# Kernel tuning notes

Measured on AMD Instinct MI355X. Metric: run time of the kernel, lower is better.

The kernel has to match this reference:

```python
import jax, jax.numpy as jnp
import numpy as np

E, L, R, H, V = 8, 8, 4, 4096, 32000
B, S = 2, 1024


def setup_inputs() -> dict:
    key = jax.random.key(0)
    ks = jax.random.split(key, 8)
    scale = 0.02
    return {
        "hidden_state": jax.random.normal(ks[0], (B, S, H), jnp.float32),
        "router_w": jax.random.normal(ks[1], (E, H), jnp.float32) * scale,
        "router_b": jnp.zeros((E,), jnp.float32),
        "expert_B": jax.random.normal(ks[2], (E, L, R, H), jnp.float32) * scale,
        "expert_A": jax.random.normal(ks[3], (E, L, H, R), jnp.float32) * scale,
        "deep_B": jax.random.normal(ks[4], (L, R, H), jnp.float32) * scale,
        "deep_A": jax.random.normal(ks[5], (L, H, R), jnp.float32) * scale,
        "lm_head_w": jax.random.normal(ks[6], (V, H), jnp.float32) * scale,
    }


def reference(hidden_state, router_w, router_b, expert_B, expert_A,
              deep_B, deep_A, lm_head_w):
    h = hidden_state  # [B,S,H]
    # Router applies softmax internally; forward softmaxes AGAIN (faithful to source).
    router_logits = jax.nn.softmax(
        jnp.einsum('bsh,eh->bse', h, router_w) + router_b, axis=-1)
    router_probs = jax.nn.softmax(router_logits, axis=-1)  # [B,S,E]
    psum = jnp.sum(router_probs, axis=-1, keepdims=True)   # [B,S,1] (== 1)

    n_layers = deep_B.shape[0]
    for i in range(n_layers):
        # All experts' LoRA low-rank projections in one batched contraction.
        z = jnp.einsum('bsh,erh->bser', h, expert_B[:, i])  # [B,S,E,r]
        # combined = sum_e p_e * (h + z_e @ A_e^T) = h * sum_e p_e + weighted delta
        zw = z * router_probs[..., None]                    # [B,S,E,r]
        delta = jnp.einsum('bser,ehr->bsh', zw, expert_A[:, i])
        combined = h * psum + delta                         # [B,S,H]
        # Residual deep LoRA merge: x + (x @ B^T) @ A^T
        low = jnp.einsum('bsh,rh->bsr', combined, deep_B[i])
        h = combined + jnp.einsum('bsr,hr->bsh', low, deep_A[i])

    lm_logits = jnp.einsum('bsh,vh->bsv', h, lm_head_w)  # [B,S,V]
    return (lm_logits, router_logits)
```

## Files before the change

### kernel.cpp

```cpp
#include <hip/hip_runtime.h>
#include <cstdint>
#include <cstddef>

#define HD 4096
#define EE 8
#define LL 8
#define RR 4
#define VV 32000
#define NTOK 2048
#define NKT (HD / 64)
#define T8 8

typedef __attribute__((ext_vector_type(8))) short bf16x8;
typedef __attribute__((ext_vector_type(4))) float f32x4;
typedef __attribute__((ext_vector_type(4))) unsigned short u16x4;

static __device__ __forceinline__ unsigned short f2bf(float f) {
    unsigned int u = __builtin_bit_cast(unsigned int, f);
    unsigned int r = (u + 0x7FFFu + ((u >> 16) & 1u)) >> 16;
    return (unsigned short)r;
}

__global__ __launch_bounds__(1024, 4) void fused_layers(
    const float* __restrict__ h_in,
    const float* __restrict__ router_w,
    const float* __restrict__ router_b,
    const float* __restrict__ expert_B,
    const float* __restrict__ expert_A,
    const float* __restrict__ deep_B,
    const float* __restrict__ deep_A,
    float* __restrict__ router_logits,
    unsigned short* __restrict__ h_out)
{
    __shared__ float h_lds[T8][HD];
    __shared__ float zw_lds[T8][32];
    __shared__ float probs_lds[T8][EE];
    __shared__ float psum_lds[T8];
    __shared__ float red[16][T8][4];
    __shared__ float low_lds[T8][4];

    const int tid  = threadIdx.x;
    const int lane = tid & 63;
    const int wv   = tid >> 6;
    const int t0   = blockIdx.x * T8;

    for (int t = 0; t < T8; ++t)
        ((float4*)h_lds[t])[tid] = ((const float4*)(h_in + (size_t)(t0 + t) * HD))[tid];
    __syncthreads();

    if (wv < T8) {
        float racc[EE];
        #pragma unroll
        for (int e = 0; e < EE; ++e) racc[e] = 0.f;
        const float4* h4 = (const float4*)h_lds[wv];
        for (int k4 = 0; k4 < HD / 256; ++k4) {
            int idx = lane + k4 * 64;
            float4 hv = h4[idx];
            #pragma unroll
            for (int e = 0; e < EE; ++e) {
                float4 w4 = ((const float4*)(router_w + e * HD))[idx];
                racc[e] += w4.x * hv.x + w4.y * hv.y + w4.z * hv.z + w4.w * hv.w;
            }
        }
        #pragma unroll
        for (int e = 0; e < EE; ++e)
            for (int m = 1; m < 64; m <<= 1) racc[e] += __shfl_xor(racc[e], m);
        if (lane == 0) {
            float lg[EE], mx = -1e30f;
            #pragma unroll
            for (int e = 0; e < EE; ++e) { lg[e] = racc[e] + router_b[e]; mx = fmaxf(mx, lg[e]); }
            float s = 0.f;
            #pragma unroll
            for (int e = 0; e < EE; ++e) { lg[e] = expf(lg[e] - mx); s += lg[e]; }
            float inv = 1.f / s;
            float p1[EE], mx2 = -1e30f;
            #pragma unroll
            for (int e = 0; e < EE; ++e) { p1[e] = lg[e] * inv; mx2 = fmaxf(mx2, p1[e]); }
            float s2 = 0.f, q2[EE];
            #pragma unroll
            for (int e = 0; e < EE; ++e) { q2[e] = expf(p1[e] - mx2); s2 += q2[e]; }
            float inv2 = 1.f / s2, ps = 0.f;
            #pragma unroll
            for (int e = 0; e < EE; ++e) {
                float p2 = q2[e] * inv2;
                probs_lds[wv][e] = p2;
                ps += p2;
                router_logits[(size_t)(t0 + wv) * EE + e] = p1[e];
            }
            psum_lds[wv] = ps;
        }
    }
    __syncthreads();

    for (int li = 0; li < LL; ++li) {
        {
            float zacc[2][T8] = {};
            const float4* bp4[2];
            #pragma unroll
            for (int j = 0; j < 2; ++j) {
                int er = wv * 2 + j;
                int e = er >> 2, r = er & 3;
                bp4[j] = (const float4*)(expert_B + (size_t)((e * LL + li) * RR + r) * HD);
            }
            for (int k4 = 0; k4 < HD / 256; ++k4) {
                int idx = lane + k4 * 64;
                float4 hv[T8];
                #pragma unroll
                for (int t = 0; t < T8; ++t) hv[t] = ((const float4*)h_lds[t])[idx];
                #pragma unroll
                for (int j = 0; j < 2; ++j) {
                    float4 w4 = bp4[j][idx];
                    #pragma unroll
                    for (int t = 0; t < T8; ++t)
                        zacc[j][t] += w4.x * hv[t].x + w4.y * hv[t].y +
                                      w4.z * hv[t].z + w4.w * hv[t].w;
                }
            }
            #pragma unroll
            for (int j = 0; j < 2; ++j)
                #pragma unroll
                for (int t = 0; t < T8; ++t) {
                    float v = zacc[j][t];
                    for (int m = 1; m < 64; m <<= 1) v += __shfl_xor(v, m);
                    zacc[j][t] = v;
                }
            if (lane == 0) {
                #pragma unroll
                for (int j = 0; j < 2; ++j) {
                    int er = wv * 2 + j;
                    #pragma unroll
                    for (int t = 0; t < T8; ++t)
                        zw_lds[t][er] = zacc[j][t] * probs_lds[t][er >> 2];
                }
            }
        }
        __syncthreads();

        float dacc[T8][4] = {};
        const int pbase = wv * 256 + lane;
        for (int e = 0; e < EE; ++e) {
            float zwt[T8][4];
            #pragma unroll
            for (int t = 0; t < T8; ++t)
                #pragma unroll
                for (int r = 0; r < RR; ++r) zwt[t][r] = zw_lds[t][e * 4 + r];
            const float4* ap = (const float4*)expert_A + (size_t)(e * LL + li) * HD;
            #pragma unroll
            for (int it = 0; it < 4; ++it) {
                float4 a4 = ap[pbase + it * 64];
                #pragma unroll
                for (int t = 0; t < T8; ++t)
                    dacc[t][it] += zwt[t][0] * a4.x + zwt[t][1] * a4.y +
                                   zwt[t][2] * a4.z + zwt[t][3] * a4.w;
            }
        }

        float lowacc[T8][4] = {};
        float psv[T8];
        #pragma unroll
        for (int t = 0; t < T8; ++t) psv[t] = psum_lds[t];
        const float* dbp = deep_B + (size_t)li * (RR * HD);
        #pragma unroll
        for (int it = 0; it < 4; ++it) {
            int pos = pbase + it * 64;
            float db0 = dbp[pos], db1 = dbp[HD + pos], db2 = dbp[2 * HD + pos], db3 = dbp[3 * HD + pos];
            #pragma unroll
            for (int t = 0; t < T8; ++t) {
                float c = h_lds[t][pos] * psv[t] + dacc[t][it];
                h_lds[t][pos] = c;
                lowacc[t][0] += c * db0; lowacc[t][1] += c * db1;
                lowacc[t][2] += c * db2; lowacc[t][3] += c * db3;
            }
        }
        #pragma unroll
        for (int t = 0; t < T8; ++t)
            #pragma unroll
            for (int r = 0; r < RR; ++r) {
                float v = lowacc[t][r];
                for (int m = 1; m < 64; m <<= 1) v += __shfl_xor(v, m);
                lowacc[t][r] = v;
            }
        if (lane == 0) {
            #pragma unroll
            for (int t = 0; t < T8; ++t)
                #pragma unroll
                for (int r = 0; r < RR; ++r) red[wv][t][r] = lowacc[t][r];
        }
        __syncthreads();
        if (tid < 32) {
            int t = tid >> 2, r = tid & 3;
            float s = 0.f;
            #pragma unroll
            for (int w = 0; w < 16; ++w) s += red[w][t][r];
            low_lds[t][r] = s;
        }
        __syncthreads();

        {
            float lw[T8][4];
            #pragma unroll
            for (int t = 0; t < T8; ++t)
                #pragma unroll
                for (int r = 0; r < RR; ++r) lw[t][r] = low_lds[t][r];
            const float4* dap = (const float4*)deep_A + (size_t)li * HD;
            #pragma unroll
            for (int it = 0; it < 4; ++it) {
                int pos = pbase + it * 64;
                float4 a4 = dap[pos];
                #pragma unroll
                for (int t = 0; t < T8; ++t)
                    h_lds[t][pos] += lw[t][0] * a4.x + lw[t][1] * a4.y +
                                     lw[t][2] * a4.z + lw[t][3] * a4.w;
            }
        }
        __syncthreads();
    }

    for (int t = 0; t < T8; ++t) {
        float4 v = ((const float4*)h_lds[t])[tid];
        ushort4 o;
        o.x = f2bf(v.x); o.y = f2bf(v.y); o.z = f2bf(v.z); o.w = f2bf(v.w);
        ((ushort4*)(h_out + (size_t)(t0 + t) * HD))[tid] = o;
    }
}

__global__ __launch_bounds__(256) void cvt_kernel(const f32x4* __restrict__ in,
                                                  u16x4* __restrict__ out, int n4)
{
    int i = blockIdx.x * 256 + threadIdx.x;
    int stride = gridDim.x * 256;
    for (; i < n4; i += stride) {
        f32x4 v = __builtin_nontemporal_load(&in[i]);
        u16x4 o;
        o.x = f2bf(v.x); o.y = f2bf(v.y); o.z = f2bf(v.z); o.w = f2bf(v.w);
        __builtin_nontemporal_store(o, &out[i]);
    }
}

#define GLD(src, dst) __builtin_amdgcn_global_load_lds( \
    (const __attribute__((address_space(1))) unsigned int*)(src), \
    (__attribute__((address_space(3))) unsigned int*)(dst), 16, 0, 0)

#define STAGE(pp, matoff, bufv, hh, ktv) do { \
    char* db_ = smem + (bufv) * 65536 + (matoff) + (hh) * 16384 + wv * 1024; \
    GLD(pp[0] + (size_t)(hh) * (128ull * HD * 2) + (size_t)(ktv) * 128, db_); \
    GLD(pp[1] + (size_t)(hh) * (128ull * HD * 2) + (size_t)(ktv) * 128, db_ + 8192); \
} while (0)

#define LDSREAD(off) (*(const bf16x8*)(smem + (off)))

__global__ __launch_bounds__(512, 2) void lm_gemm256(
    const unsigned short* __restrict__ A,
    const unsigned short* __restrict__ Bw,
    float* __restrict__ C)
{
    __shared__ __attribute__((aligned(128))) char smem[131072];

    const int bid = blockIdx.x;
    const int swz = (bid & 7) * 125 + (bid >> 3);
    const int bm = swz & 7;
    const int bn = swz >> 3;

    const int tid  = threadIdx.x;
    const int lane = tid & 63;
    const int wv   = tid >> 6;
    const int wr   = wv >> 2;
    const int wc   = wv & 3;

    const char* pA[2];
    const char* pB[2];
    #pragma unroll
    for (int q = 0; q < 2; ++q) {
        int off = (q * 512 + tid) * 16;
        int p = off ^ (((off >> 9) & 1) << 5);
        int st = p >> 10;
        int r  = (st >> 1) * 16 + ((p >> 6) & 15);
        int cb = (st & 1) * 64 + (p & 63);
        pA[q] = (const char*)(A  + (size_t)(bm * 256 + r) * HD) + cb;
        pB[q] = (const char*)(Bw + (size_t)(bn * 256 + r) * HD) + cb;
    }

    const int xlane = ((lane >> 3) & 1) << 5;
    const int abase = ((wr * 8) << 11) + ((lane & 15) << 6) + ((lane >> 4) << 4);
    const int bbase = 32768 + ((wc * 4) << 11) + ((lane & 15) << 6) + ((lane >> 4) << 4);

    f32x4 acc[8][4] = {};
    bf16x8 aF[4][2], bF0[2][2][2], bF1[2][2];

    STAGE(pB, 32768, 0, 0, 0);
    STAGE(pB, 32768, 0, 1, 0);
    STAGE(pA, 0,     0, 0, 0);
    STAGE(pA, 0,     0, 1, 0);
    STAGE(pB, 32768, 1, 0, 1);
    STAGE(pB, 32768, 1, 1, 1);
    asm volatile("s_waitcnt vmcnt(4)" ::: "memory");
    __builtin_amdgcn_s_barrier();
    __builtin_amdgcn_sched_barrier(0);
    #pragma unroll
    for (int n = 0; n < 2; ++n)
        #pragma unroll
        for (int ks = 0; ks < 2; ++ks)
            bF0[0][n][ks] = LDSREAD(((bbase + (n << 11) + (ks << 10)) ^ xlane));

    #pragma unroll 2
    for (int kt = 0; kt < NKT; ++kt) {
        const int cur = kt & 1;
        const int oth = cur ^ 1;
        const int cb0 = cur << 16;

        #pragma unroll
        for (int i = 0; i < 4; ++i)
            #pragma unroll
            for (int ks = 0; ks < 2; ++ks)
                aF[i][ks] = LDSREAD(cb0 + ((abase + (i << 11) + (ks << 10)) ^ xlane));
        if (kt + 1 < NKT) STAGE(pA, 0, oth, 0, kt + 1);
        __builtin_amdgcn_s_barrier();
        __builtin_amdgcn_sched_barrier(0);
        __builtin_amdgcn_s_setprio(1);
        #pragma unroll
        for (int ks = 0; ks < 2; ++ks)
            #pragma unroll
            for (int i = 0; i < 4; ++i)
                #pragma unroll
                for (int n = 0; n < 2; ++n)
                    acc[i][n] = __builtin_amdgcn_mfma_f32_16x16x32_bf16(
                        aF[i][ks], bF0[cur][n][ks], acc[i][n], 0, 0, 0);
        __builtin_amdgcn_s_setprio(0);
        __builtin_amdgcn_s_barrier();
        __builtin_amdgcn_sched_barrier(0);

        #pragma unroll
        for (int n = 0; n < 2; ++n)
            #pragma unroll
            for (int ks = 0; ks < 2; ++ks)
                bF1[n][ks] = LDSREAD(cb0 + ((bbase + ((n + 2) << 11) + (ks << 10)) ^ xlane));
        if (kt + 1 < NKT) STAGE(pA, 0, oth, 1, kt + 1);
        __builtin_amdgcn_s_barrier();
        __builtin_amdgcn_sched_barrier(0);
        __builtin_amdgcn_s_setprio(1);
        #pragma unroll
        for (int ks = 0; ks < 2; ++ks)
            #pragma unroll
            for (int i = 0; i < 4; ++i)
                #pragma unroll
                for (int n = 0; n < 2; ++n)
                    acc[i][n + 2] = __builtin_amdgcn_mfma_f32_16x16x32_bf16(
                        aF[i][ks], bF1[n][ks], acc[i][n + 2], 0, 0, 0);
        __builtin_amdgcn_s_setprio(0);
        __builtin_amdgcn_s_barrier();
        __builtin_amdgcn_sched_barrier(0);

        #pragma unroll
        for (int i = 0; i < 4; ++i)
            #pragma unroll
            for (int ks = 0; ks < 2; ++ks)
                aF[i][ks] = LDSREAD(cb0 + ((abase + ((i + 4) << 11) + (ks << 10)) ^ xlane));
        if (kt + 2 < NKT) STAGE(pB, 32768, cur, 0, kt + 2);
        __builtin_amdgcn_s_barrier();
        __builtin_amdgcn_sched_barrier(0);
        __builtin_amdgcn_s_setprio(1);
        #pragma unroll
        for (int ks = 0; ks < 2; ++ks)
            #pragma unroll
            for (int i = 0; i < 4; ++i)
                #pragma unroll
                for (int n = 0; n < 2; ++n)
                    acc[i + 4][n + 2] = __builtin_amdgcn_mfma_f32_16x16x32_bf16(
                        aF[i][ks], bF1[n][ks], acc[i + 4][n + 2], 0, 0, 0);
        __builtin_amdgcn_s_setprio(0);
        __builtin_amdgcn_s_barrier();
        __builtin_amdgcn_sched_barrier(0);

        if (kt + 2 < NKT) {
            STAGE(pB, 32768, cur, 1, kt + 2);
            asm volatile("s_waitcnt vmcnt(4)" ::: "memory");
        } else {
            asm volatile("s_waitcnt vmcnt(0)" ::: "memory");
        }
        __builtin_amdgcn_s_barrier();
        __builtin_amdgcn_sched_barrier(0);
        if (kt + 1 < NKT) {
            const int nb0 = oth << 16;
            #pragma unroll
            for (int n = 0; n < 2; ++n)
                #pragma unroll
                for (int ks = 0; ks < 2; ++ks)
                    bF0[oth][n][ks] = LDSREAD(nb0 + ((bbase + (n << 11) + (ks << 10)) ^ xlane));
        }
        __builtin_amdgcn_s_setprio(1);
        #pragma unroll
        for (int ks = 0; ks < 2; ++ks)
            #pragma unroll
            for (int i = 0; i < 4; ++i)
                #pragma unroll
                for (int n = 0; n < 2; ++n)
                    acc[i + 4][n] = __builtin_amdgcn_mfma_f32_16x16x32_bf16(
                        aF[i][ks], bF0[cur][n][ks], acc[i + 4][n], 0, 0, 0);
        __builtin_amdgcn_s_setprio(0);
        __builtin_amdgcn_s_barrier();
        __builtin_amdgcn_sched_barrier(0);
    }

    const int crow0 = bm * 256 + wr * 128 + ((lane >> 4) << 2);
    const int ccol0 = bn * 256 + wc * 64 + (lane & 15);
    #pragma unroll
    for (int fm = 0; fm < 8; ++fm)
        #pragma unroll
        for (int fn = 0; fn < 4; ++fn) {
            int row = crow0 + fm * 16;
            int col = ccol0 + fn * 16;
            #pragma unroll
            for (int j = 0; j < 4; ++j)
                C[(size_t)(row + j) * VV + col] = acc[fm][fn][j];
        }
}

extern "C" void kernel_launch(void* const* d_in, const int* in_sizes, int n_in,
                              void* d_out, int out_size, void* d_ws, size_t ws_size,
                              hipStream_t stream) {
    const float* h_in      = (const float*)d_in[0];
    const float* router_w  = (const float*)d_in[1];
    const float* router_b  = (const float*)d_in[2];
    const float* expert_B  = (const float*)d_in[3];
    const float* expert_A  = (const float*)d_in[4];
    const float* deep_B    = (const float*)d_in[5];
    const float* deep_A    = (const float*)d_in[6];
    const float* lm_head_w = (const float*)d_in[7];

    float* out = (float*)d_out;
    float* router_logits_out = out + (size_t)NTOK * VV;

    unsigned short* h_bf = (unsigned short*)d_ws;
    unsigned short* w_bf = (unsigned short*)((char*)d_ws + (size_t)NTOK * HD * 2);

    fused_layers<<<dim3(NTOK / T8), dim3(1024), 0, stream>>>(
        h_in, router_w, router_b, expert_B, expert_A, deep_B, deep_A,
        router_logits_out, h_bf);

    cvt_kernel<<<dim3(4096), dim3(256), 0, stream>>>(
        (const f32x4*)lm_head_w, (u16x4*)w_bf, VV * HD / 4);

    lm_gemm256<<<dim3((NTOK / 256) * (VV / 256)), dim3(512), 0, stream>>>(
        h_bf, w_bf, out);
}
```

Baseline: 908.3 us.

## Fuse lm_head bf16 conversion into layer kernel to overlap with latency-bound work

Removes the separate fp32-to-bf16 conversion kernel for the lm_head weight and spreads the conversion in chunks across the layer loop of the fused layers kernel. Each block converts a slice between its barrier phases, so the bandwidth-heavy conversion overlaps the latency-bound per-token LoRA math and one launch goes away. The risk is memory traffic contention slowing the layer phases and extra register pressure in an already large kernel.

```diff
diff --git a/kernel.cpp b/kernel.cpp
--- a/kernel.cpp
+++ b/kernel.cpp
@@ -10,6 +10,7 @@
 #define NTOK 2048
 #define NKT (HD / 64)
 #define T8 8
+#define N4 (VV * HD / 4)
 
 typedef __attribute__((ext_vector_type(8))) short bf16x8;
 typedef __attribute__((ext_vector_type(4))) float f32x4;
@@ -21,7 +22,22 @@
     return (unsigned short)r;
 }
 
-__global__ __launch_bounds__(1024, 4) void fused_layers(
+#define CVT_CHUNK(c) do { \
+    size_t base_ = ((size_t)(li * 4 + (c)) * 256 + blockIdx.x) * 4096; \
+    _Pragma("unroll") \
+    for (int q_ = 0; q_ < 4; ++q_) { \
+        size_t i_ = base_ + q_ * 1024 + tid; \
+        if (i_ < (size_t)N4) { \
+            f32x4 v_ = __builtin_nontemporal_load(&lm_w[i_]); \
+            u16x4 o_; \
+            o_.x = f2bf(v_.x); o_.y = f2bf(v_.y); \
+            o_.z = f2bf(v_.z); o_.w = f2bf(v_.w); \
+            __builtin_nontemporal_store(o_, &w_bf[i_]); \
+        } \
+    } \
+} while (0)
+
+__global__ __launch_bounds__(1024, 4) void fused_layers_cvt(
     const float* __restrict__ h_in,
     const float* __restrict__ router_w,
     const float* __restrict__ router_b,
@@ -30,7 +46,9 @@
     const float* __restrict__ deep_B,
     const float* __restrict__ deep_A,
     float* __restrict__ router_logits,
-    unsigned short* __restrict__ h_out)
+    unsigned short* __restrict__ h_out,
+    const f32x4* __restrict__ lm_w,
+    u16x4* __restrict__ w_bf)
 {
     __shared__ float h_lds[T8][HD];
     __shared__ float zw_lds[T8][32];
@@ -93,6 +111,7 @@
     __syncthreads();
 
     for (int li = 0; li < LL; ++li) {
+        CVT_CHUNK(0);
         {
             float zacc[2][T8] = {};
             const float4* bp4[2];
@@ -135,6 +154,7 @@
             }
         }
         __syncthreads();
+        CVT_CHUNK(1);
 
         float dacc[T8][4] = {};
         const int pbase = wv * 256 + lane;
@@ -195,6 +215,7 @@
             low_lds[t][r] = s;
         }
         __syncthreads();
+        CVT_CHUNK(2);
 
         {
             float lw[T8][4];
@@ -214,6 +235,7 @@
             }
         }
         __syncthreads();
+        CVT_CHUNK(3);
     }
 
     for (int t = 0; t < T8; ++t) {
@@ -221,19 +243,6 @@
         ushort4 o;
         o.x = f2bf(v.x); o.y = f2bf(v.y); o.z = f2bf(v.z); o.w = f2bf(v.w);
         ((ushort4*)(h_out + (size_t)(t0 + t) * HD))[tid] = o;
-    }
-}
-
-__global__ __launch_bounds__(256) void cvt_kernel(const f32x4* __restrict__ in,
-                                                  u16x4* __restrict__ out, int n4)
-{
-    int i = blockIdx.x * 256 + threadIdx.x;
-    int stride = gridDim.x * 256;
-    for (; i < n4; i += stride) {
-        f32x4 v = __builtin_nontemporal_load(&in[i]);
-        u16x4 o;
-        o.x = f2bf(v.x); o.y = f2bf(v.y); o.z = f2bf(v.z); o.w = f2bf(v.w);
-        __builtin_nontemporal_store(o, &out[i]);
     }
 }
 
@@ -433,12 +442,9 @@
     unsigned short* h_bf = (unsigned short*)d_ws;
     unsigned short* w_bf = (unsigned short*)((char*)d_ws + (size_t)NTOK * HD * 2);
 
-    fused_layers<<<dim3(NTOK / T8), dim3(1024), 0, stream>>>(
+    fused_layers_cvt<<<dim3(NTOK / T8), dim3(1024), 0, stream>>>(
         h_in, router_w, router_b, expert_B, expert_A, deep_B, deep_A,
-        router_logits_out, h_bf);
-
-    cvt_kernel<<<dim3(4096), dim3(256), 0, stream>>>(
-        (const f32x4*)lm_head_w, (u16x4*)w_bf, VV * HD / 4);
+        router_logits_out, h_bf, (const f32x4*)lm_head_w, (u16x4*)w_bf);
 
     lm_gemm256<<<dim3((NTOK / 256) * (VV / 256)), dim3(512), 0, stream>>>(
         h_bf, w_bf, out);
```

After: 902.8 us. About the same (-0.6%).
